# Kernel tuning notes

Hardware: AMD Instinct MI355X
Metric: run time of the kernel (lower is better)

The kernel has to match this reference:

```python
import jax, jax.numpy as jnp
import numpy as np

ROWS, COLS, N_CHARS = 384, 768, 69  # CHARSET length = 69
CH, CW = 28, 14  # char tile height, width


def setup_inputs() -> dict:
    key = jax.random.key(0)
    k1, k2 = jax.random.split(key)
    grid_logits = jax.random.normal(k1, (ROWS, COLS, N_CHARS), dtype=jnp.float32)
    # font rasterizations are in [0, 1] (pixel intensity / 255)
    font = jax.random.uniform(k2, (N_CHARS, CH, CW), dtype=jnp.float32)
    return {"grid_logits": grid_logits, "font": font}


def reference(grid_logits, font):
    rows, cols, n_chars = grid_logits.shape
    ch, cw = font.shape[1], font.shape[2]
    # softmax over characters per grid cell
    probs = jax.nn.softmax(grid_logits, axis=-1)  # (R, C, N)
    # soft blend of font tiles: (R, C, ch, cw)
    soft_tiles = jnp.einsum('rcn,nhw->rchw', probs, font)
    # assemble full image: equivalent to nested torch.cat over rows/cols
    soft_image = soft_tiles.transpose(0, 2, 1, 3).reshape(rows * ch, cols * cw)
    return soft_image[None, None]  # (1, 1, H, W)
```

## Files before the change

### kernel.cpp

```cpp
#include <hip/hip_runtime.h>
#include <hip/hip_bf16.h>

#define ROWS 384
#define COLS 768
#define NCH  69
#define CH   28
#define CW   14
#define KP   96
#define IMG_W 10752
#define ROW_U 104

typedef __attribute__((ext_vector_type(8))) short bfrag;
typedef __attribute__((ext_vector_type(4))) float f32x4;

__device__ __forceinline__ unsigned bf16bits(float x) {
    unsigned b = __float_as_uint(x);
    b += 0x7FFFu + ((b >> 16) & 1u);
    return b >> 16;
}

__global__ __launch_bounds__(256)
void font_prep(const float* __restrict__ font, unsigned short* __restrict__ Fh) {
    int idx = blockIdx.x * 256 + threadIdx.x;
    if (idx >= CH * 16 * KP) return;
    int k  = idx % KP;
    int hw = idx / KP;
    int w  = hw % 16, h = hw / 16;
    float v = (w < CW && k < NCH) ? font[k * (CH * CW) + h * CW + w] : 0.f;
    Fh[idx] = (unsigned short)bf16bits(v);
}

__global__ __launch_bounds__(128, 3)
void diffrender_v11(const float* __restrict__ logits,
                    const unsigned short* __restrict__ Fh,
                    float* __restrict__ out)
{
    __shared__ __align__(16) unsigned short smem[2][64 * ROW_U];

    const int tid  = threadIdx.x;
    const int lane = tid & 63;
    const int wv   = tid >> 6;
    const int cell = blockIdx.x * 128 + tid;
    const int r    = blockIdx.x / 6;
    const int cb   = (blockIdx.x % 6) * 128;

    const float* lp = logits + (size_t)cell * NCH;
    float e[NCH];
    float m = -INFINITY;
#pragma unroll
    for (int n = 0; n < NCH; ++n) { e[n] = lp[n]; m = fmaxf(m, e[n]); }
    float s = 0.f;
#pragma unroll
    for (int n = 0; n < NCH; ++n) { e[n] = __expf(e[n] - m); s += e[n]; }
    const float inv = 1.f / s;

    unsigned* prow = (unsigned*)&smem[wv][(size_t)lane * ROW_U];
#pragma unroll
    for (int i = 0; i < 34; ++i)
        prow[i] = bf16bits(e[2 * i] * inv) | (bf16bits(e[2 * i + 1] * inv) << 16);
    prow[34] = bf16bits(e[68] * inv);
#pragma unroll
    for (int i = 35; i < 48; ++i) prow[i] = 0;

    const int w15   = lane & 15;
    const int kgrp  = (lane >> 4) * 8;
    const int crow4 = (lane >> 4) * 4;
    bfrag a[4][3];
#pragma unroll
    for (int mt = 0; mt < 4; ++mt)
#pragma unroll
        for (int ks = 0; ks < 3; ++ks)
            a[mt][ks] = *(const bfrag*)&smem[wv][(size_t)(mt * 16 + w15) * ROW_U + ks * 32 + kgrp];

    float* stage = (float*)&smem[wv][0];

    const unsigned short* fb = Fh + (size_t)w15 * KP + kgrp;
    bfrag bcur[2][3], bnxt[2][3];
#pragma unroll
    for (int hh = 0; hh < 2; ++hh)
#pragma unroll
        for (int ks = 0; ks < 3; ++ks)
            bcur[hh][ks] = *(const bfrag*)(fb + (size_t)(hh * 16) * KP + ks * 32);

#pragma unroll 1
    for (int h2 = 0; h2 < CH / 2; ++h2) {
        const int h = 2 * h2;
        if (h2 + 1 < CH / 2) {
            const unsigned short* fn = fb + (size_t)((h + 2) * 16) * KP;
#pragma unroll
            for (int hh = 0; hh < 2; ++hh)
#pragma unroll
                for (int ks = 0; ks < 3; ++ks)
                    bnxt[hh][ks] = *(const bfrag*)(fn + (size_t)(hh * 16) * KP + ks * 32);
        }

        f32x4 acc[2][4];
#pragma unroll
        for (int hh = 0; hh < 2; ++hh)
#pragma unroll
            for (int mt = 0; mt < 4; ++mt)
                acc[hh][mt] = f32x4{0, 0, 0, 0};
#pragma unroll
        for (int hh = 0; hh < 2; ++hh)
#pragma unroll
            for (int mt = 0; mt < 4; ++mt)
#pragma unroll
                for (int ks = 0; ks < 3; ++ks)
                    acc[hh][mt] = __builtin_amdgcn_mfma_f32_16x16x32_bf16(
                        a[mt][ks], bcur[hh][ks], acc[hh][mt], 0, 0, 0);

        if (w15 < CW) {
#pragma unroll
            for (int hh = 0; hh < 2; ++hh)
#pragma unroll
                for (int mt = 0; mt < 4; ++mt)
#pragma unroll
                    for (int j = 0; j < 4; ++j)
                        stage[hh * 896 + (mt * 16 + crow4 + j) * CW + w15] = acc[hh][mt][j];
        }

#pragma unroll
        for (int hh = 0; hh < 2; ++hh) {
            f32x4* o4 = (f32x4*)(out + (size_t)(r * CH + h + hh) * IMG_W
                                     + (size_t)(cb + wv * 64) * CW);
            const f32x4* s4 = (const f32x4*)(stage + hh * 896);
#pragma unroll
            for (int i = 0; i < 4; ++i) {
                const int idx = i * 64 + lane;
                if (idx < 224) __builtin_nontemporal_store(s4[idx], &o4[idx]);
            }
        }

#pragma unroll
        for (int hh = 0; hh < 2; ++hh)
#pragma unroll
            for (int ks = 0; ks < 3; ++ks)
                bcur[hh][ks] = bnxt[hh][ks];
    }
}

extern "C" void kernel_launch(void* const* d_in, const int* in_sizes, int n_in,
                              void* d_out, int out_size, void* d_ws, size_t ws_size,
                              hipStream_t stream) {
    const float* logits = (const float*)d_in[0];
    const float* font   = (const float*)d_in[1];
    float* out          = (float*)d_out;
    unsigned short* Fh  = (unsigned short*)d_ws;

    font_prep<<<(CH * 16 * KP + 255) / 256, 256, 0, stream>>>(font, Fh);

    const int blocks = (ROWS * COLS) / 128;
    diffrender_v11<<<blocks, 128, 0, stream>>>(logits, Fh, out);
}
```

Baseline: 107.9 us.

## Split softmax into separate kernel writing bf16 probabilities to workspace

Moves the per-cell softmax and bf16 packing into its own kernel, which writes padded 72-element probability rows to workspace. The render kernel then loads these rows with vector loads into a smaller shared-memory buffer and runs the MFMA blend. The third K-slice fragment reads the same address for every lane group; this stays correct because the matching font entries are zero. The aim is to separate the register-heavy softmax from the MFMA/store loop so each kernel can be tuned on its own. The cost is an extra round trip of roughly 42 MB of intermediate data through HBM and one more launch. The old fused kernel is kept as a fallback when the workspace is too small.

```diff
diff --git a/kernel.cpp b/kernel.cpp
--- a/kernel.cpp
+++ b/kernel.cpp
@@ -8,7 +8,11 @@
 #define CW   14
 #define KP   96
 #define IMG_W 10752
-#define ROW_U 104
+#define ROW_U 72
+#define ROW_U_F 104
+#define FH_ELems (CH * 16 * KP)
+#define PROB_OFF 131072
+#define PROBS_BYTES (294912ull * ROW_U * 2)
 
 typedef __attribute__((ext_vector_type(8))) short bfrag;
 typedef __attribute__((ext_vector_type(4))) float f32x4;
@@ -22,7 +26,7 @@
 __global__ __launch_bounds__(256)
 void font_prep(const float* __restrict__ font, unsigned short* __restrict__ Fh) {
     int idx = blockIdx.x * 256 + threadIdx.x;
-    if (idx >= CH * 16 * KP) return;
+    if (idx >= FH_ELems) return;
     int k  = idx % KP;
     int hw = idx / KP;
     int w  = hw % 16, h = hw / 16;
@@ -30,10 +34,37 @@
     Fh[idx] = (unsigned short)bf16bits(v);
 }
 
+__global__ __launch_bounds__(256)
+void softmax_probs(const float* __restrict__ logits,
+                   unsigned short* __restrict__ probs) {
+    const int cell = blockIdx.x * 256 + threadIdx.x;
+    const float* lp = logits + (size_t)cell * NCH;
+    float e[NCH];
+    float m = -INFINITY;
+#pragma unroll
+    for (int n = 0; n < NCH; ++n) { e[n] = lp[n]; m = fmaxf(m, e[n]); }
+    float s = 0.f;
+#pragma unroll
+    for (int n = 0; n < NCH; ++n) { e[n] = __expf(e[n] - m); s += e[n]; }
+    const float inv = 1.f / s;
+
+    unsigned pk[ROW_U / 2];
+#pragma unroll
+    for (int i = 0; i < 34; ++i)
+        pk[i] = bf16bits(e[2 * i] * inv) | (bf16bits(e[2 * i + 1] * inv) << 16);
+    pk[34] = bf16bits(e[68] * inv);
+    pk[35] = 0;
+
+    uint4* dst = (uint4*)(probs + (size_t)cell * ROW_U);
+#pragma unroll
+    for (int i = 0; i < 9; ++i)
+        dst[i] = make_uint4(pk[4 * i], pk[4 * i + 1], pk[4 * i + 2], pk[4 * i + 3]);
+}
+
 __global__ __launch_bounds__(128, 3)
-void diffrender_v11(const float* __restrict__ logits,
-                    const unsigned short* __restrict__ Fh,
-                    float* __restrict__ out)
+void render_v14(const unsigned short* __restrict__ probs,
+                const unsigned short* __restrict__ Fh,
+                float* __restrict__ out)
 {
     __shared__ __align__(16) unsigned short smem[2][64 * ROW_U];
 
@@ -44,6 +75,108 @@
     const int r    = blockIdx.x / 6;
     const int cb   = (blockIdx.x % 6) * 128;
 
+    const bfrag* gp = (const bfrag*)(probs + (size_t)cell * ROW_U);
+    bfrag tmp[9];
+#pragma unroll
+    for (int i = 0; i < 9; ++i) tmp[i] = gp[i];
+    bfrag* lrow = (bfrag*)&smem[wv][(size_t)lane * ROW_U];
+#pragma unroll
+    for (int i = 0; i < 9; ++i) lrow[i] = tmp[i];
+
+    const int w15   = lane & 15;
+    const int g     = lane >> 4;
+    const int kgrp  = g * 8;
+    const int crow4 = g * 4;
+    bfrag a[4][3];
+#pragma unroll
+    for (int mt = 0; mt < 4; ++mt) {
+        const size_t base = (size_t)(mt * 16 + w15) * ROW_U;
+        a[mt][0] = *(const bfrag*)&smem[wv][base + kgrp];
+        a[mt][1] = *(const bfrag*)&smem[wv][base + 32 + kgrp];
+        a[mt][2] = *(const bfrag*)&smem[wv][base + 64];
+    }
+
+    float* stage = (float*)&smem[wv][0];
+
+    const unsigned short* fb = Fh + (size_t)w15 * KP + kgrp;
+    bfrag bcur[2][3], bnxt[2][3];
+#pragma unroll
+    for (int hh = 0; hh < 2; ++hh)
+#pragma unroll
+        for (int ks = 0; ks < 3; ++ks)
+            bcur[hh][ks] = *(const bfrag*)(fb + (size_t)(hh * 16) * KP + ks * 32);
+
+#pragma unroll 1
+    for (int h2 = 0; h2 < CH / 2; ++h2) {
+        const int h = 2 * h2;
+        if (h2 + 1 < CH / 2) {
+            const unsigned short* fn = fb + (size_t)((h + 2) * 16) * KP;
+#pragma unroll
+            for (int hh = 0; hh < 2; ++hh)
+#pragma unroll
+                for (int ks = 0; ks < 3; ++ks)
+                    bnxt[hh][ks] = *(const bfrag*)(fn + (size_t)(hh * 16) * KP + ks * 32);
+        }
+
+        f32x4 acc[2][4];
+#pragma unroll
+        for (int hh = 0; hh < 2; ++hh)
+#pragma unroll
+            for (int mt = 0; mt < 4; ++mt)
+                acc[hh][mt] = f32x4{0, 0, 0, 0};
+#pragma unroll
+        for (int hh = 0; hh < 2; ++hh)
+#pragma unroll
+            for (int mt = 0; mt < 4; ++mt)
+#pragma unroll
+                for (int ks = 0; ks < 3; ++ks)
+                    acc[hh][mt] = __builtin_amdgcn_mfma_f32_16x16x32_bf16(
+                        a[mt][ks], bcur[hh][ks], acc[hh][mt], 0, 0, 0);
+
+        if (w15 < CW) {
+#pragma unroll
+            for (int hh = 0; hh < 2; ++hh)
+#pragma unroll
+                for (int mt = 0; mt < 4; ++mt)
+#pragma unroll
+                    for (int j = 0; j < 4; ++j)
+                        stage[hh * 896 + (mt * 16 + crow4 + j) * CW + w15] = acc[hh][mt][j];
+        }
+
+#pragma unroll
+        for (int hh = 0; hh < 2; ++hh) {
+            f32x4* o4 = (f32x4*)(out + (size_t)(r * CH + h + hh) * IMG_W
+                                     + (size_t)(cb + wv * 64) * CW);
+            const f32x4* s4 = (const f32x4*)(stage + hh * 896);
+#pragma unroll
+            for (int i = 0; i < 4; ++i) {
+                const int idx = i * 64 + lane;
+                if (idx < 224) __builtin_nontemporal_store(s4[idx], &o4[idx]);
+            }
+        }
+
+#pragma unroll
+        for (int hh = 0; hh < 2; ++hh)
+#pragma unroll
+            for (int ks = 0; ks < 3; ++ks)
+                bcur[hh][ks] = bnxt[hh][ks];
+    }
+}
+
+__global__ __launch_bounds__(128, 3)
+void diffrender_mono(const float* __restrict__ logits,
+                     const unsigned short* __restrict__ Fh,
+                     float* __restrict__ out)
+{
+    __shared__ __align__(16) unsigned short smem[2][64 * ROW_U_F];
+
+    const int tid  = threadIdx.x;
+    const int lane = tid & 63;
+    const int wv   = tid >> 6;
+    const int cell = blockIdx.x * 128 + tid;
+    const int r    = blockIdx.x / 6;
+    const int cb   = (blockIdx.x % 6) * 128;
+
     const float* lp = logits + (size_t)cell * NCH;
     float e[NCH];
     float m = -INFINITY;
@@ -54,7 +187,7 @@
     for (int n = 0; n < NCH; ++n) { e[n] = __expf(e[n] - m); s += e[n]; }
     const float inv = 1.f / s;
 
-    unsigned* prow = (unsigned*)&smem[wv][(size_t)lane * ROW_U];
+    unsigned* prow = (unsigned*)&smem[wv][(size_t)lane * ROW_U_F];
 #pragma unroll
     for (int i = 0; i < 34; ++i)
         prow[i] = bf16bits(e[2 * i] * inv) | (bf16bits(e[2 * i + 1] * inv) << 16);
@@ -70,7 +203,7 @@
     for (int mt = 0; mt < 4; ++mt)
 #pragma unroll
         for (int ks = 0; ks < 3; ++ks)
-            a[mt][ks] = *(const bfrag*)&smem[wv][(size_t)(mt * 16 + w15) * ROW_U + ks * 32 + kgrp];
+            a[mt][ks] = *(const bfrag*)&smem[wv][(size_t)(mt * 16 + w15) * ROW_U_F + ks * 32 + kgrp];
 
     float* stage = (float*)&smem[wv][0];
 
@@ -147,8 +280,14 @@
     float* out          = (float*)d_out;
     unsigned short* Fh  = (unsigned short*)d_ws;
 
-    font_prep<<<(CH * 16 * KP + 255) / 256, 256, 0, stream>>>(font, Fh);
-
-    const int blocks = (ROWS * COLS) / 128;
-    diffrender_v11<<<blocks, 128, 0, stream>>>(logits, Fh, out);
-}
+    font_prep<<<(FH_ELems + 255) / 256, 256, 0, stream>>>(font, Fh);
+
+    const size_t need = PROB_OFF + PROBS_BYTES;
+    if (ws_size >= need) {
+        unsigned short* probs = (unsigned short*)((char*)d_ws + PROB_OFF);
+        softmax_probs<<<(ROWS * COLS) / 256, 256, 0, stream>>>(logits, probs);
+        render_v14<<<(ROWS * COLS) / 128, 128, 0, stream>>>(probs, Fh, out);
+    } else {
+        diffrender_mono<<<(ROWS * COLS) / 128, 128, 0, stream>>>(logits, Fh, out);
+    }
+}
```

Measured after the change: 131.0 us. 21.4% more time.
